# Performance work log

Measured on AMD Instinct MI355X. Metric: run time of the kernel, lower is better.

Reference implementation:

```python
import jax, jax.numpy as jnp
import numpy as np

N_NODES = 100000
N_EDGES = 1600000
F_IN = 512
D_EMB = 128
D_HID = 64
N_CLS = 32
EPS = 1e-5


def setup_inputs() -> dict:
    key = jax.random.key(0)
    ks = jax.random.split(key, 16)
    def w(k, shape):
        fan_in = shape[0]
        return jax.random.normal(k, shape, dtype=jnp.float32) / jnp.sqrt(jnp.float32(fan_in))
    return {
        "x": jax.random.normal(ks[0], (N_NODES, F_IN), dtype=jnp.float32),
        "W1": w(ks[1], (F_IN, D_EMB)), "b1": jnp.zeros((D_EMB,), jnp.float32),
        "Wc1": w(ks[2], (D_EMB, D_HID)), "bc1": jnp.zeros((D_HID,), jnp.float32),
        "Wc2": w(ks[3], (D_HID, D_HID)), "bc2": jnp.zeros((D_HID,), jnp.float32),
        "Wc3": w(ks[4], (D_HID, D_HID)), "bc3": jnp.zeros((D_HID,), jnp.float32),
        "gamma": jnp.ones((D_HID,), jnp.float32), "beta": jnp.zeros((D_HID,), jnp.float32),
        "W2": w(ks[5], (D_HID, N_CLS)), "b2": jnp.zeros((N_CLS,), jnp.float32),
        "W3": w(ks[6], (N_CLS, N_CLS)), "b3": jnp.zeros((N_CLS,), jnp.float32),
        "edge_index": jax.random.randint(ks[7], (2, N_EDGES), 0, N_NODES, dtype=jnp.int32),
    }


def _agg_mean(h, src, dst, n):
    # gather source-node features along edges, sum into destination nodes, divide by degree
    s = jax.ops.segment_sum(h[src], dst, num_segments=n)          # [N, d]
    deg = jax.ops.segment_sum(jnp.ones((src.shape[0], 1), h.dtype), dst, num_segments=n)
    return s / jnp.maximum(deg, 1.0)


def _conv1p(h, src, dst, W, b):
    # ConvolutionalLayer_1P: neighborhood gather/aggregate -> linear -> relu
    return jax.nn.relu(_agg_mean(h, src, dst, h.shape[0]) @ W + b)


def reference(x, W1, b1, Wc1, bc1, Wc2, bc2, Wc3, bc3, gamma, beta, W2, b2, W3, b3, edge_index):
    src, dst = edge_index[0], edge_index[1]
    # linmaps1 on 0th-order ptensors == identity copy
    h = jax.nn.relu(x @ W1 + b1)                 # lin1 + relu (dropout = identity in eval)
    h = _conv1p(h, src, dst, Wc1, bc1)           # conv1
    h = _conv1p(h, src, dst, Wc2, bc2)           # conv2
    h = _conv1p(h, src, dst, Wc3, bc3)           # conv3
    mean = jnp.mean(h, axis=0)
    var = jnp.var(h, axis=0)
    h = (h - mean) * jax.lax.rsqrt(var + EPS) * gamma + beta  # batchnorm (batch stats)
    h = jax.nn.relu(h @ W2 + b2)                 # lin2 + relu (dropout = identity)
    out = h @ W3 + b3                            # lin3; linmaps0 == identity
    return out
```

## Files before the change

kernel.cpp:

```cpp
#include <hip/hip_runtime.h>
#include <cstdint>
#include <cstddef>

constexpr int F_IN  = 512;
constexpr int D_EMB = 128;
constexpr int D_HID = 64;
constexpr int N_CLS = 32;

typedef __attribute__((ext_vector_type(8))) short short8;
typedef __attribute__((ext_vector_type(4))) float floatx4;

__device__ inline unsigned short f2bf(float f) {
  union { float f; uint32_t u; } v; v.f = f;
  uint32_t r = v.u + 0x7FFF + ((v.u >> 16) & 1);
  return (unsigned short)(r >> 16);
}

__global__ __launch_bounds__(256) void wt_kernel(
    const float* __restrict__ W1, short8* __restrict__ Wt2)
{
  int idx = blockIdx.x * 256 + threadIdx.x;
  int kc8 = idx >> 10, lin = idx & 1023;
  int ct = lin >> 7, rem = lin & 127, ks = rem >> 6, ln = rem & 63;
  int col = ct * 16 + (ln & 15);
  int k0 = kc8 * 64 + ks * 32 + (ln >> 4) * 8;
  short8 s;
#pragma unroll
  for (int j = 0; j < 8; ++j)
    s[j] = (short)f2bf(W1[(size_t)(k0 + j) * D_EMB + col]);
  Wt2[idx] = s;
}

__global__ __launch_bounds__(256) void l1c1_kernel(
    const float* __restrict__ X, const short8* __restrict__ Wt2,
    const float* __restrict__ b1, const float* __restrict__ Wc1,
    float* __restrict__ P, int n)
{
  __shared__ __align__(16) char smem[50176];
  short8* Xs = (short8*)smem;
  short8* Ws = (short8*)(smem + 8192);
  float (*Hs)[132] = (float(*)[132])smem;
  float (*Wc)[64]  = (float(*)[64])(smem + 33792);

  const int t = threadIdx.x;
  const int wave = t >> 6, lane = t & 63;
  const int quad = lane >> 4, mrow = lane & 15;
  const int node0 = blockIdx.x * 64;
  const int cw = wave * 2;

  float4 wp[4];
#pragma unroll
  for (int i = 0; i < 4; ++i) wp[i] = ((const float4*)Wc1)[i * 256 + t];

  const float* sp[2];
  int soff[2];
#pragma unroll
  for (int i = 0; i < 2; ++i) {
    int g = t + i * 256;
    int row = g >> 3, col8 = g & 7;
    soff[i] = row * 128 + ((col8 * 16) ^ ((row & 7) << 4));
    int gr = node0 + row; if (gr >= n) gr = n - 1;
    sp[i] = &X[(size_t)gr * F_IN + col8 * 8];
  }

  floatx4 acc[4][2];
#pragma unroll
  for (int i = 0; i < 4; ++i)
#pragma unroll
    for (int j = 0; j < 2; ++j) acc[i][j] = (floatx4){0.f, 0.f, 0.f, 0.f};

  float4 xrA[2][2], xrB[2][2];
  short8 wrA[4], wrB[4];

#pragma unroll
  for (int i = 0; i < 2; ++i) {
    xrA[i][0] = *(const float4*)sp[i];
    xrA[i][1] = *(const float4*)(sp[i] + 4);
    xrB[i][0] = *(const float4*)(sp[i] + 64);
    xrB[i][1] = *(const float4*)(sp[i] + 68);
  }
#pragma unroll
  for (int i = 0; i < 4; ++i) {
    wrA[i] = Wt2[t + i * 256];
    wrB[i] = Wt2[1024 + t + i * 256];
  }

  auto substep = [&](float4 (&xr)[2][2], short8 (&wr)[4], int knext) {
    short8 s8[2];
#pragma unroll
    for (int i = 0; i < 2; ++i) {
      s8[i][0] = (short)f2bf(xr[i][0].x); s8[i][1] = (short)f2bf(xr[i][0].y);
      s8[i][2] = (short)f2bf(xr[i][0].z); s8[i][3] = (short)f2bf(xr[i][0].w);
      s8[i][4] = (short)f2bf(xr[i][1].x); s8[i][5] = (short)f2bf(xr[i][1].y);
      s8[i][6] = (short)f2bf(xr[i][1].z); s8[i][7] = (short)f2bf(xr[i][1].w);
    }
    __syncthreads();
#pragma unroll
    for (int i = 0; i < 2; ++i)
      *(short8*)((char*)Xs + soff[i]) = s8[i];
#pragma unroll
    for (int i = 0; i < 4; ++i)
      Ws[t + i * 256] = wr[i];
    __syncthreads();

    if (knext < 8) {
#pragma unroll
      for (int i = 0; i < 2; ++i) {
        const float* p = sp[i] + knext * 64;
        xr[i][0] = *(const float4*)p;
        xr[i][1] = *(const float4*)(p + 4);
      }
#pragma unroll
      for (int i = 0; i < 4; ++i)
        wr[i] = Wt2[knext * 1024 + t + i * 256];
    }

#pragma unroll
    for (int ks = 0; ks < 2; ++ks) {
      short8 af[4], bf[2];
#pragma unroll
      for (int rt = 0; rt < 4; ++rt) {
        int row = rt * 16 + mrow;
        int byteoff = row * 128 + ((ks * 64 + quad * 16) ^ ((row & 7) << 4));
        af[rt] = *(const short8*)((const char*)Xs + byteoff);
      }
#pragma unroll
      for (int c = 0; c < 2; ++c)
        bf[c] = Ws[((cw + c) * 2 + ks) * 64 + lane];
#pragma unroll
      for (int rt = 0; rt < 4; ++rt)
#pragma unroll
        for (int c = 0; c < 2; ++c)
          acc[rt][c] = __builtin_amdgcn_mfma_f32_16x16x32_bf16(
              af[rt], bf[c], acc[rt][c], 0, 0, 0);
    }
  };

#pragma unroll 1
  for (int kc8 = 0; kc8 < 8; kc8 += 2) {
    substep(xrA, wrA, kc8 + 2);
    substep(xrB, wrB, kc8 + 3);
  }

  __syncthreads();
#pragma unroll
  for (int ct = 0; ct < 2; ++ct) {
    int col = (cw + ct) * 16 + mrow;
    float b = b1[col];
#pragma unroll
    for (int rt = 0; rt < 4; ++rt)
#pragma unroll
      for (int r = 0; r < 4; ++r)
        Hs[rt * 16 + quad * 4 + r][col] = fmaxf(acc[rt][ct][r] + b, 0.f);
  }
#pragma unroll
  for (int i = 0; i < 4; ++i)
    ((float4*)&Wc[0][0])[i * 256 + t] = wp[i];
  __syncthreads();

#pragma unroll
  for (int i = 0; i < 4; ++i)
    wp[i] = ((const float4*)Wc1)[1024 + i * 256 + t];

  const int rg = t >> 4, cg = t & 15;
  float acc2[4][4];
#pragma unroll
  for (int i = 0; i < 4; ++i)
#pragma unroll
    for (int j = 0; j < 4; ++j) acc2[i][j] = 0.f;

#pragma unroll 8
  for (int k = 0; k < 64; ++k) {
    float a[4] = {Hs[rg*4+0][k], Hs[rg*4+1][k], Hs[rg*4+2][k], Hs[rg*4+3][k]};
    float4 b = *(const float4*)&Wc[k][cg * 4];
#pragma unroll
    for (int i = 0; i < 4; ++i) {
      acc2[i][0] += a[i]*b.x; acc2[i][1] += a[i]*b.y;
      acc2[i][2] += a[i]*b.z; acc2[i][3] += a[i]*b.w;
    }
  }
  __syncthreads();
#pragma unroll
  for (int i = 0; i < 4; ++i)
    ((float4*)&Wc[0][0])[i * 256 + t] = wp[i];
  __syncthreads();

#pragma unroll 8
  for (int k = 0; k < 64; ++k) {
    float a[4] = {Hs[rg*4+0][64+k], Hs[rg*4+1][64+k],
                  Hs[rg*4+2][64+k], Hs[rg*4+3][64+k]};
    float4 b = *(const float4*)&Wc[k][cg * 4];
#pragma unroll
    for (int i = 0; i < 4; ++i) {
      acc2[i][0] += a[i]*b.x; acc2[i][1] += a[i]*b.y;
      acc2[i][2] += a[i]*b.z; acc2[i][3] += a[i]*b.w;
    }
  }
#pragma unroll
  for (int i = 0; i < 4; ++i) {
    int gn = node0 + rg * 4 + i;
    if (gn < n) {
      float4 o = make_float4(acc2[i][0], acc2[i][1], acc2[i][2], acc2[i][3]);
      *(float4*)&P[(size_t)gn * 64 + cg * 4] = o;
    }
  }
}

__device__ inline float gather_row(
    const float* __restrict__ P, const int* __restrict__ adj,
    int beg, int end, int lane)
{
  float a0=0.f,a1=0.f,a2=0.f,a3=0.f,a4=0.f,a5=0.f,a6=0.f,a7=0.f;
  int j = beg;
  for (; j + 8 <= end; j += 8) {
    int s0=adj[j+0], s1=adj[j+1], s2=adj[j+2], s3=adj[j+3];
    int s4=adj[j+4], s5=adj[j+5], s6=adj[j+6], s7=adj[j+7];
    a0 += P[(size_t)s0 * 64 + lane];
    a1 += P[(size_t)s1 * 64 + lane];
    a2 += P[(size_t)s2 * 64 + lane];
    a3 += P[(size_t)s3 * 64 + lane];
    a4 += P[(size_t)s4 * 64 + lane];
    a5 += P[(size_t)s5 * 64 + lane];
    a6 += P[(size_t)s6 * 64 + lane];
    a7 += P[(size_t)s7 * 64 + lane];
  }
  if (j < end) {
    int e1 = end - 1;
    int s0 = adj[j];
    int s1 = adj[min(j+1,e1)], s2 = adj[min(j+2,e1)], s3 = adj[min(j+3,e1)];
    int s4 = adj[min(j+4,e1)], s5 = adj[min(j+5,e1)], s6 = adj[min(j+6,e1)];
    float v0 = P[(size_t)s0 * 64 + lane];
    float v1 = P[(size_t)s1 * 64 + lane];
    float v2 = P[(size_t)s2 * 64 + lane];
    float v3 = P[(size_t)s3 * 64 + lane];
    float v4 = P[(size_t)s4 * 64 + lane];
    float v5 = P[(size_t)s5 * 64 + lane];
    float v6 = P[(size_t)s6 * 64 + lane];
    a0 += v0;
    a1 += (j+1 < end) ? v1 : 0.f;
    a2 += (j+2 < end) ? v2 : 0.f;
    a3 += (j+3 < end) ? v3 : 0.f;
    a4 += (j+4 < end) ? v4 : 0.f;
    a5 += (j+5 < end) ? v5 : 0.f;
    a6 += (j+6 < end) ? v6 : 0.f;
  }
  return ((a0+a1)+(a2+a3))+((a4+a5)+(a6+a7));
}

__global__ __launch_bounds__(512) void gmm_kernel(
    const float* __restrict__ P, const int* __restrict__ offs,
    const int* __restrict__ adj, const int* __restrict__ deg,
    const float* __restrict__ bin, const float* __restrict__ W,
    float* __restrict__ Out, int n)
{
  __shared__ float Hs[64][68];
  __shared__ float Ws[64][64];
  const int t = threadIdx.x;
  const int wave = t >> 6, lane = t & 63;
  const int node0 = blockIdx.x * 64;

#pragma unroll
  for (int i = 0; i < 2; ++i) {
    int lin = t + i * 512;
    ((float4*)&Ws[0][0])[lin] = ((const float4*)W)[lin];
  }
  const float bb = bin[lane];

#pragma unroll 1
  for (int nd = 0; nd < 8; ++nd) {
    int ln = wave * 8 + nd;
    int node = node0 + ln;
    float v = 0.f;
    if (node < n) {
      int beg = __builtin_amdgcn_readfirstlane(offs[node]);
      int end = __builtin_amdgcn_readfirstlane(offs[node + 1]);
      float s = gather_row(P, adj, beg, end, lane);
      float rd = 1.f / fmaxf((float)deg[node], 1.f);
      v = fmaxf(s * rd + bb, 0.f);
    }
    Hs[ln][lane] = v;
  }
  __syncthreads();

  const int rg = t >> 4, cg = t & 15;
  float acc[2][4];
#pragma unroll
  for (int i = 0; i < 2; ++i)
#pragma unroll
    for (int j = 0; j < 4; ++j) acc[i][j] = 0.f;

#pragma unroll 8
  for (int k = 0; k < 64; ++k) {
    float a[2] = {Hs[rg * 2 + 0][k], Hs[rg * 2 + 1][k]};
    float4 b = *(const float4*)&Ws[k][cg * 4];
#pragma unroll
    for (int i = 0; i < 2; ++i) {
      acc[i][0] += a[i]*b.x; acc[i][1] += a[i]*b.y;
      acc[i][2] += a[i]*b.z; acc[i][3] += a[i]*b.w;
    }
  }
#pragma unroll
  for (int i = 0; i < 2; ++i) {
    int gn = node0 + rg * 2 + i;
    if (gn < n) {
      float4 o = make_float4(acc[i][0], acc[i][1], acc[i][2], acc[i][3]);
      *(float4*)&Out[(size_t)gn * 64 + cg * 4] = o;
    }
  }
}

__global__ __launch_bounds__(512) void gp_kernel(
    const float* __restrict__ P, const int* __restrict__ offs,
    const int* __restrict__ adj, const int* __restrict__ deg,
    const float* __restrict__ bc3, float* __restrict__ H4,
    float* __restrict__ stats, int n)
{
  const int t = threadIdx.x;
  const int wave = t >> 6, lane = t & 63;
  const int node0 = blockIdx.x * 64;
  const float bb = bc3[lane];
  float s = 0.f, s2 = 0.f;

#pragma unroll 1
  for (int nd = 0; nd < 8; ++nd) {
    int node = node0 + wave * 8 + nd;
    if (node >= n) break;
    int beg = __builtin_amdgcn_readfirstlane(offs[node]);
    int end = __builtin_amdgcn_readfirstlane(offs[node + 1]);
    float a = gather_row(P, adj, beg, end, lane);
    float rd = 1.f / fmaxf((float)deg[node], 1.f);
    float v = fmaxf(a * rd + bb, 0.f);
    H4[(size_t)node * 64 + lane] = v;
    s += v; s2 += v * v;
  }

  __shared__ float red[2][8][64];
  red[0][wave][lane] = s; red[1][wave][lane] = s2;
  __syncthreads();
  if (t < 128) {
    int which = t >> 6, ff = t & 63;
    float a = 0.f;
#pragma unroll
    for (int w = 0; w < 8; ++w) a += red[which][w][ff];
    atomicAdd(&stats[which * 64 + ff], a);
  }
}

__global__ __launch_bounds__(256) void hist_kernel(
    const int* __restrict__ dst, int* __restrict__ G,
    float* __restrict__ stats, int nE, int B, int NB)
{
  __shared__ int h[256];
  int blk = blockIdx.x, t = threadIdx.x;
  if (blk == 0 && t < 128) stats[t] = 0.f;
  h[t] = 0;
  __syncthreads();
  int base = blk * 8192;
  int lim = min(8192, nE - base);
  for (int i = t; i < lim; i += 256)
    atomicAdd(&h[dst[base + i] >> 9], 1);
  __syncthreads();
  if (t < NB) G[t * B + blk] = h[t];
}

__global__ __launch_bounds__(256) void scan1_kernel(
    const int* __restrict__ in, int* __restrict__ out,
    int* __restrict__ bsum, int n)
{
  __shared__ int sh[256];
  int t = threadIdx.x;
  int i = blockIdx.x * 256 + t;
  int c = (i < n) ? in[i] : 0;
  sh[t] = c;
  __syncthreads();
#pragma unroll
  for (int off = 1; off < 256; off <<= 1) {
    int v = 0;
    if (t >= off) v = sh[t - off];
    __syncthreads();
    if (t >= off) sh[t] += v;
    __syncthreads();
  }
  if (i < n) out[i] = sh[t] - c;
  if (t == 255) bsum[blockIdx.x] = sh[255];
}

__global__ __launch_bounds__(256) void scan2_kernel(int* __restrict__ bsum, int nb)
{
  __shared__ int sh[256];
  __shared__ int carry;
  int t = threadIdx.x;
  if (t == 0) carry = 0;
  __syncthreads();
  for (int base = 0; base < nb; base += 256) {
    int i = base + t;
    int v = (i < nb) ? bsum[i] : 0;
    sh[t] = v;
    __syncthreads();
#pragma unroll
    for (int off = 1; off < 256; off <<= 1) {
      int u = 0;
      if (t >= off) u = sh[t - off];
      __syncthreads();
      if (t >= off) sh[t] += u;
      __syncthreads();
    }
    int c0 = carry;
    int incl = sh[t], total = sh[255];
    if (i < nb) bsum[i] = c0 + incl - v;
    __syncthreads();
    if (t == 0) carry = c0 + total;
    __syncthreads();
  }
  if (t == 0) bsum[nb] = carry;
}

__global__ __launch_bounds__(256) void scatter2_kernel(
    const int* __restrict__ src, const int* __restrict__ dst,
    const int* __restrict__ W, const int* __restrict__ bsum,
    int2* __restrict__ EP, int nE, int B, int NB)
{
  __shared__ int cur[256];
  int blk = blockIdx.x, t = threadIdx.x;
  if (t < NB) {
    int gi = t * B + blk;
    cur[t] = W[gi] + bsum[gi >> 8];
  }
  __syncthreads();
  int base = blk * 8192;
  int lim = min(8192, nE - base);
  for (int i = t; i < lim; i += 256) {
    int s = src[base + i], d = dst[base + i];
    int slot = atomicAdd(&cur[d >> 9], 1);
    EP[slot] = make_int2(s, d);
  }
}

__global__ __launch_bounds__(256) void fillc_kernel(
    const int2* __restrict__ EP, const int* __restrict__ W,
    const int* __restrict__ bsum,
    int* __restrict__ cnt, int* __restrict__ offs, int* __restrict__ adj,
    int n, int nE, int B, int NB)
{
  __shared__ int h[512];
  int b = blockIdx.x, t = threadIdx.x;
  int g0i = b * B;
  int segStart = W[g0i] + bsum[g0i >> 8];
  int segEnd = (b == NB - 1) ? nE : (W[g0i + B] + bsum[(g0i + B) >> 8]);
  int nodeBase = b << 9;

  h[t] = 0; h[t + 256] = 0;
  __syncthreads();
  for (int i = segStart + t; i < segEnd; i += 256)
    atomicAdd(&h[EP[i].y - nodeBase], 1);
  __syncthreads();
  int c0 = h[t], c1 = h[t + 256];
#pragma unroll
  for (int off = 1; off < 512; off <<= 1) {
    int a = (t >= off) ? h[t - off] : 0;
    int bb = (t + 256 >= off) ? h[t + 256 - off] : 0;
    __syncthreads();
    h[t] += a; h[t + 256] += bb;
    __syncthreads();
  }
  int e0 = h[t] - c0, e1 = h[t + 256] - c1;
  int g0 = nodeBase + t, g1 = nodeBase + t + 256;
  if (g0 < n) { cnt[g0] = c0; offs[g0] = segStart + e0; }
  if (g1 < n) { cnt[g1] = c1; offs[g1] = segStart + e1; }
  if (b == 0 && t == 0) offs[n] = nE;
  __syncthreads();
  h[t] = e0; h[t + 256] = e1;
  __syncthreads();
  for (int i = segStart + t; i < segEnd; i += 256) {
    int2 p = EP[i];
    int slot = atomicAdd(&h[p.y - nodeBase], 1);
    adj[segStart + slot] = p.x;
  }
}

__global__ __launch_bounds__(256) void fold_kernel(
    const float* __restrict__ stats, const float* __restrict__ gamma,
    const float* __restrict__ beta, const float* __restrict__ W2,
    const float* __restrict__ b2, float* __restrict__ W2f,
    float* __restrict__ b2f, int n)
{
  __shared__ float rsg[64], corr[64];
  int t = threadIdx.x;
  if (t < 64) {
    float m = stats[t] / (float)n;
    float var = stats[64 + t] / (float)n - m * m;
    float rs = rsqrtf(var + 1e-5f);
    float g = gamma[t] * rs;
    rsg[t] = g;
    corr[t] = beta[t] - m * g;
  }
  __syncthreads();
#pragma unroll
  for (int i = 0; i < 8; ++i) {
    int lin = t + i * 256;
    int k = lin >> 5;
    W2f[lin] = rsg[k] * W2[lin];
  }
  if (t < 32) {
    float a = b2[t];
    for (int k = 0; k < 64; ++k) a += corr[k] * W2[k * 32 + t];
    b2f[t] = a;
  }
}

__global__ __launch_bounds__(256) void final_kernel(
    const float* __restrict__ H4, const float* __restrict__ W2f,
    const float* __restrict__ b2f, const float* __restrict__ W3,
    const float* __restrict__ b3, float* __restrict__ Out, int n)
{
  __shared__ float Hs[64][68];
  __shared__ float W2s[64][32];
  __shared__ float W3s[32][32];
  __shared__ float Us[64][36];
  __shared__ float b2s[32], b3s[32];
  const int t = threadIdx.x;
  const int node0 = blockIdx.x * 64;

#pragma unroll
  for (int i = 0; i < 4; ++i) {
    int lin = t + i * 256;
    int node = lin >> 4, kq = lin & 15;
    float4 v = make_float4(0.f, 0.f, 0.f, 0.f);
    if (node0 + node < n)
      v = *(const float4*)&H4[(size_t)(node0 + node) * 64 + kq * 4];
    *(float4*)&Hs[node][kq * 4] = v;
  }
#pragma unroll
  for (int i = 0; i < 2; ++i) {
    int lin = t + i * 256;
    ((float4*)&W2s[0][0])[lin] = ((const float4*)W2f)[lin];
  }
  ((float4*)&W3s[0][0])[t & 255] = ((const float4*)W3)[t & 255];
  if (t < 32) { b2s[t] = b2f[t]; b3s[t] = b3[t]; }
  __syncthreads();

  const int rg = t >> 4, cg = t & 15;
  float acc[4][2] = {{0.f,0.f},{0.f,0.f},{0.f,0.f},{0.f,0.f}};
#pragma unroll 8
  for (int k = 0; k < 64; ++k) {
    float a[4] = {Hs[rg*4+0][k], Hs[rg*4+1][k], Hs[rg*4+2][k], Hs[rg*4+3][k]};
    float w0 = W2s[k][cg*2], w1 = W2s[k][cg*2+1];
#pragma unroll
    for (int i = 0; i < 4; ++i) { acc[i][0] += a[i]*w0; acc[i][1] += a[i]*w1; }
  }
#pragma unroll
  for (int i = 0; i < 4; ++i) {
    Us[rg*4+i][cg*2+0] = fmaxf(acc[i][0] + b2s[cg*2+0], 0.f);
    Us[rg*4+i][cg*2+1] = fmaxf(acc[i][1] + b2s[cg*2+1], 0.f);
  }
  __syncthreads();

  float acc2[4][2] = {{0.f,0.f},{0.f,0.f},{0.f,0.f},{0.f,0.f}};
#pragma unroll
  for (int k = 0; k < 32; ++k) {
    float a[4] = {Us[rg*4+0][k], Us[rg*4+1][k], Us[rg*4+2][k], Us[rg*4+3][k]};
    float w0 = W3s[k][cg*2], w1 = W3s[k][cg*2+1];
#pragma unroll
    for (int i = 0; i < 4; ++i) { acc2[i][0] += a[i]*w0; acc2[i][1] += a[i]*w1; }
  }
  float (*Os)[36] = (float(*)[36])Hs;
#pragma unroll
  for (int i = 0; i < 4; ++i) {
    Os[rg*4+i][cg*2+0] = acc2[i][0] + b3s[cg*2+0];
    Os[rg*4+i][cg*2+1] = acc2[i][1] + b3s[cg*2+1];
  }
  __syncthreads();
#pragma unroll
  for (int i = 0; i < 2; ++i) {
    int lin = t + i * 256;
    int node = lin >> 3, c4 = lin & 7;
    if (node0 + node < n)
      *(float4*)&Out[(size_t)(node0 + node) * 32 + c4 * 4] =
          *(float4*)&Os[node][c4 * 4];
  }
}

extern "C" void kernel_launch(void* const* d_in, const int* in_sizes, int n_in,
                              void* d_out, int out_size, void* d_ws, size_t ws_size,
                              hipStream_t stream)
{
  const float* X     = (const float*)d_in[0];
  const float* W1    = (const float*)d_in[1];
  const float* b1    = (const float*)d_in[2];
  const float* Wc1   = (const float*)d_in[3];
  const float* bc1   = (const float*)d_in[4];
  const float* Wc2   = (const float*)d_in[5];
  const float* bc2   = (const float*)d_in[6];
  const float* Wc3   = (const float*)d_in[7];
  const float* bc3   = (const float*)d_in[8];
  const float* gamma = (const float*)d_in[9];
  const float* beta  = (const float*)d_in[10];
  const float* W2    = (const float*)d_in[11];
  const float* b2    = (const float*)d_in[12];
  const float* W3    = (const float*)d_in[13];
  const float* b3    = (const float*)d_in[14];
  const int*   ei    = (const int*)d_in[15];

  const int n  = in_sizes[0] / F_IN;
  const int nE = in_sizes[15] / 2;
  const int* src  = ei;
  const int* dstv = ei + nE;

  const int NB = (n + 511) >> 9;
  const int B  = (nE + 8191) >> 13;
  const int NG = NB * B;
  const int nbG = (NG + 255) / 256;

  float* ws    = (float*)d_ws;
  float* Pa    = ws;
  float* Pb    = Pa + (size_t)n * D_HID;
  float* stats = Pb + (size_t)n * D_HID;
  float* W2f   = stats + 128;
  float* b2f   = W2f + 2048;
  int*   cnt   = (int*)(b2f + 32);
  int*   offs  = cnt + n;
  int*   G     = offs + n + 1;
  int*   W     = G + NG;
  int*   bsum  = W + NG + 1;
  int*   adj   = bsum + nbG + 1;
  uintptr_t epAddr = ((uintptr_t)(adj + nE) + 7) & ~(uintptr_t)7;
  int2*  EP    = (int2*)epAddr;
  short8* Wt2  = (short8*)(EP + nE);
  float* H4    = Pb;

  const int nb  = (n + 63) / 64;

  wt_kernel<<<32, 256, 0, stream>>>(W1, Wt2);
  l1c1_kernel<<<nb, 256, 0, stream>>>(X, Wt2, b1, Wc1, Pa, n);

  hist_kernel<<<B, 256, 0, stream>>>(dstv, G, stats, nE, B, NB);
  scan1_kernel<<<nbG, 256, 0, stream>>>(G, W, bsum, NG);
  scan2_kernel<<<1, 256, 0, stream>>>(bsum, nbG);
  scatter2_kernel<<<B, 256, 0, stream>>>(src, dstv, W, bsum, EP, nE, B, NB);
  fillc_kernel<<<NB, 256, 0, stream>>>(EP, W, bsum, cnt, offs, adj, n, nE, B, NB);

  gmm_kernel<<<nb, 512, 0, stream>>>(Pa, offs, adj, cnt, bc1, Wc2, Pb, n);

  gmm_kernel<<<nb, 512, 0, stream>>>(Pb, offs, adj, cnt, bc2, Wc3, Pa, n);

  gp_kernel<<<nb, 512, 0, stream>>>(Pa, offs, adj, cnt, bc3, H4, stats, n);

  fold_kernel<<<1, 256, 0, stream>>>(stats, gamma, beta, W2, b2, W2f, b2f, n);
  final_kernel<<<nb, 256, 0, stream>>>(H4, W2f, b2f, W3, b3, (float*)d_out, n);
}
```

Baseline: 632.0 us.

## Store intermediate node features as bf16 and split gathers across half-waves

The projected node features feeding the first two aggregation passes are now stored in bf16, which halves the bytes moved by the random per-edge gathers. Each gather now has two half-waves take alternate edges, with each lane loading two features, and the partial sums are combined with a cross-lane shuffle. The CSR offsets for each block are staged in shared memory. The third pass keeps fp32 input, so the workspace layout changes. The cost is bf16 rounding error in the intermediate activations, which could affect accuracy tolerance.

```diff
diff --git a/kernel.cpp b/kernel.cpp
--- a/kernel.cpp
+++ b/kernel.cpp
@@ -14,6 +14,10 @@
   union { float f; uint32_t u; } v; v.f = f;
   uint32_t r = v.u + 0x7FFF + ((v.u >> 16) & 1);
   return (unsigned short)(r >> 16);
+}
+
+__device__ inline uint32_t pack2bf(float lo, float hi) {
+  return ((uint32_t)f2bf(hi) << 16) | (uint32_t)f2bf(lo);
 }
 
 __global__ __launch_bounds__(256) void wt_kernel(
@@ -34,7 +38,7 @@
 __global__ __launch_bounds__(256) void l1c1_kernel(
     const float* __restrict__ X, const short8* __restrict__ Wt2,
     const float* __restrict__ b1, const float* __restrict__ Wc1,
-    float* __restrict__ P, int n)
+    unsigned short* __restrict__ P, int n)
 {
   __shared__ __align__(16) char smem[50176];
   short8* Xs = (short8*)smem;
@@ -200,63 +204,75 @@
   for (int i = 0; i < 4; ++i) {
     int gn = node0 + rg * 4 + i;
     if (gn < n) {
-      float4 o = make_float4(acc2[i][0], acc2[i][1], acc2[i][2], acc2[i][3]);
-      *(float4*)&P[(size_t)gn * 64 + cg * 4] = o;
-    }
-  }
-}
-
-__device__ inline float gather_row(
+      uint2 o;
+      o.x = pack2bf(acc2[i][0], acc2[i][1]);
+      o.y = pack2bf(acc2[i][2], acc2[i][3]);
+      *(uint2*)&P[(size_t)gn * 64 + cg * 4] = o;
+    }
+  }
+}
+
+__device__ inline void gather2_bf(
+    const unsigned short* __restrict__ P, const int* __restrict__ adj,
+    int beg, int end, int g, int li, float& c0, float& c1)
+{
+  c0 = 0.f; c1 = 0.f;
+  if (end <= beg) return;
+  int e1 = end - 1;
+  for (int jj = beg + g; jj < end; jj += 16) {
+#pragma unroll
+    for (int k = 0; k < 8; ++k) {
+      int e = jj + 2 * k;
+      int ec = min(e, e1);
+      int idx = adj[ec];
+      uint32_t u = *(const uint32_t*)&P[(size_t)idx * 64 + li * 2];
+      float lo = __uint_as_float(u << 16);
+      float hi = __uint_as_float(u & 0xFFFF0000u);
+      bool p = e < end;
+      c0 += p ? lo : 0.f;
+      c1 += p ? hi : 0.f;
+    }
+  }
+  c0 += __shfl_xor(c0, 32, 64);
+  c1 += __shfl_xor(c1, 32, 64);
+}
+
+__device__ inline void gather2_f32(
     const float* __restrict__ P, const int* __restrict__ adj,
-    int beg, int end, int lane)
-{
-  float a0=0.f,a1=0.f,a2=0.f,a3=0.f,a4=0.f,a5=0.f,a6=0.f,a7=0.f;
-  int j = beg;
-  for (; j + 8 <= end; j += 8) {
-    int s0=adj[j+0], s1=adj[j+1], s2=adj[j+2], s3=adj[j+3];
-    int s4=adj[j+4], s5=adj[j+5], s6=adj[j+6], s7=adj[j+7];
-    a0 += P[(size_t)s0 * 64 + lane];
-    a1 += P[(size_t)s1 * 64 + lane];
-    a2 += P[(size_t)s2 * 64 + lane];
-    a3 += P[(size_t)s3 * 64 + lane];
-    a4 += P[(size_t)s4 * 64 + lane];
-    a5 += P[(size_t)s5 * 64 + lane];
-    a6 += P[(size_t)s6 * 64 + lane];
-    a7 += P[(size_t)s7 * 64 + lane];
-  }
-  if (j < end) {
-    int e1 = end - 1;
-    int s0 = adj[j];
-    int s1 = adj[min(j+1,e1)], s2 = adj[min(j+2,e1)], s3 = adj[min(j+3,e1)];
-    int s4 = adj[min(j+4,e1)], s5 = adj[min(j+5,e1)], s6 = adj[min(j+6,e1)];
-    float v0 = P[(size_t)s0 * 64 + lane];
-    float v1 = P[(size_t)s1 * 64 + lane];
-    float v2 = P[(size_t)s2 * 64 + lane];
-    float v3 = P[(size_t)s3 * 64 + lane];
-    float v4 = P[(size_t)s4 * 64 + lane];
-    float v5 = P[(size_t)s5 * 64 + lane];
-    float v6 = P[(size_t)s6 * 64 + lane];
-    a0 += v0;
-    a1 += (j+1 < end) ? v1 : 0.f;
-    a2 += (j+2 < end) ? v2 : 0.f;
-    a3 += (j+3 < end) ? v3 : 0.f;
-    a4 += (j+4 < end) ? v4 : 0.f;
-    a5 += (j+5 < end) ? v5 : 0.f;
-    a6 += (j+6 < end) ? v6 : 0.f;
-  }
-  return ((a0+a1)+(a2+a3))+((a4+a5)+(a6+a7));
-}
-
+    int beg, int end, int g, int li, float& c0, float& c1)
+{
+  c0 = 0.f; c1 = 0.f;
+  if (end <= beg) return;
+  int e1 = end - 1;
+  for (int jj = beg + g; jj < end; jj += 16) {
+#pragma unroll
+    for (int k = 0; k < 8; ++k) {
+      int e = jj + 2 * k;
+      int ec = min(e, e1);
+      int idx = adj[ec];
+      float2 u = *(const float2*)&P[(size_t)idx * 64 + li * 2];
+      bool p = e < end;
+      c0 += p ? u.x : 0.f;
+      c1 += p ? u.y : 0.f;
+    }
+  }
+  c0 += __shfl_xor(c0, 32, 64);
+  c1 += __shfl_xor(c1, 32, 64);
+}
+
+template<bool INBF, bool OUTBF>
 __global__ __launch_bounds__(512) void gmm_kernel(
-    const float* __restrict__ P, const int* __restrict__ offs,
+    const void* __restrict__ Pv, const int* __restrict__ offs,
     const int* __restrict__ adj, const int* __restrict__ deg,
     const float* __restrict__ bin, const float* __restrict__ W,
-    float* __restrict__ Out, int n)
+    void* __restrict__ Outv, int n)
 {
   __shared__ float Hs[64][68];
   __shared__ float Ws[64][64];
+  __shared__ int offss[65];
   const int t = threadIdx.x;
   const int wave = t >> 6, lane = t & 63;
+  const int g = lane >> 5, li = lane & 31;
   const int node0 = blockIdx.x * 64;
 
 #pragma unroll
@@ -264,21 +280,30 @@
     int lin = t + i * 512;
     ((float4*)&Ws[0][0])[lin] = ((const float4*)W)[lin];
   }
-  const float bb = bin[lane];
+  if (t < 65) offss[t] = offs[min(node0 + t, n)];
+  __syncthreads();
+
+  const float2 bb = *(const float2*)&bin[li * 2];
 
 #pragma unroll 1
   for (int nd = 0; nd < 8; ++nd) {
     int ln = wave * 8 + nd;
     int node = node0 + ln;
-    float v = 0.f;
     if (node < n) {
-      int beg = __builtin_amdgcn_readfirstlane(offs[node]);
-      int end = __builtin_amdgcn_readfirstlane(offs[node + 1]);
-      float s = gather_row(P, adj, beg, end, lane);
+      float c0, c1;
+      if (INBF)
+        gather2_bf((const unsigned short*)Pv, adj, offss[ln], offss[ln + 1],
+                   g, li, c0, c1);
+      else
+        gather2_f32((const float*)Pv, adj, offss[ln], offss[ln + 1],
+                    g, li, c0, c1);
       float rd = 1.f / fmaxf((float)deg[node], 1.f);
-      v = fmaxf(s * rd + bb, 0.f);
-    }
-    Hs[ln][lane] = v;
+      float v0 = fmaxf(c0 * rd + bb.x, 0.f);
+      float v1 = fmaxf(c1 * rd + bb.y, 0.f);
+      if (g == 0) *(float2*)&Hs[ln][li * 2] = make_float2(v0, v1);
+    } else if (g == 0) {
+      *(float2*)&Hs[ln][li * 2] = make_float2(0.f, 0.f);
+    }
   }
   __syncthreads();
 
@@ -303,8 +328,15 @@
   for (int i = 0; i < 2; ++i) {
     int gn = node0 + rg * 2 + i;
     if (gn < n) {
-      float4 o = make_float4(acc[i][0], acc[i][1], acc[i][2], acc[i][3]);
-      *(float4*)&Out[(size_t)gn * 64 + cg * 4] = o;
+      if (OUTBF) {
+        uint2 o;
+        o.x = pack2bf(acc[i][0], acc[i][1]);
+        o.y = pack2bf(acc[i][2], acc[i][3]);
+        *(uint2*)&((unsigned short*)Outv)[(size_t)gn * 64 + cg * 4] = o;
+      } else {
+        float4 o = make_float4(acc[i][0], acc[i][1], acc[i][2], acc[i][3]);
+        *(float4*)&((float*)Outv)[(size_t)gn * 64 + cg * 4] = o;
+      }
     }
   }
 }
@@ -315,27 +347,36 @@
     const float* __restrict__ bc3, float* __restrict__ H4,
     float* __restrict__ stats, int n)
 {
+  __shared__ int offss[65];
   const int t = threadIdx.x;
   const int wave = t >> 6, lane = t & 63;
+  const int g = lane >> 5, li = lane & 31;
   const int node0 = blockIdx.x * 64;
-  const float bb = bc3[lane];
-  float s = 0.f, s2 = 0.f;
+  if (t < 65) offss[t] = offs[min(node0 + t, n)];
+  __syncthreads();
+
+  const float2 bb = *(const float2*)&bc3[li * 2];
+  float s0 = 0.f, s1 = 0.f, q0 = 0.f, q1 = 0.f;
 
 #pragma unroll 1
   for (int nd = 0; nd < 8; ++nd) {
-    int node = node0 + wave * 8 + nd;
+    int ln = wave * 8 + nd;
+    int node = node0 + ln;
     if (node >= n) break;
-    int beg = __builtin_amdgcn_readfirstlane(offs[node]);
-    int end = __builtin_amdgcn_readfirstlane(offs[node + 1]);
-    float a = gather_row(P, adj, beg, end, lane);
+    float c0, c1;
+    gather2_f32(P, adj, offss[ln], offss[ln + 1], g, li, c0, c1);
     float rd = 1.f / fmaxf((float)deg[node], 1.f);
-    float v = fmaxf(a * rd + bb, 0.f);
-    H4[(size_t)node * 64 + lane] = v;
-    s += v; s2 += v * v;
+    float v0 = fmaxf(c0 * rd + bb.x, 0.f);
+    float v1 = fmaxf(c1 * rd + bb.y, 0.f);
+    if (g == 0) *(float2*)&H4[(size_t)node * 64 + li * 2] = make_float2(v0, v1);
+    s0 += v0; s1 += v1; q0 += v0 * v0; q1 += v1 * v1;
   }
 
   __shared__ float red[2][8][64];
-  red[0][wave][lane] = s; red[1][wave][lane] = s2;
+  if (g == 0) {
+    red[0][wave][li * 2 + 0] = s0; red[0][wave][li * 2 + 1] = s1;
+    red[1][wave][li * 2 + 0] = q0; red[1][wave][li * 2 + 1] = q1;
+  }
   __syncthreads();
   if (t < 128) {
     int which = t >> 6, ff = t & 63;
@@ -611,10 +652,12 @@
   const int NG = NB * B;
   const int nbG = (NG + 255) / 256;
 
-  float* ws    = (float*)d_ws;
-  float* Pa    = ws;
-  float* Pb    = Pa + (size_t)n * D_HID;
-  float* stats = Pb + (size_t)n * D_HID;
+  char* wsb = (char*)d_ws;
+  unsigned short* Pa = (unsigned short*)wsb;
+  unsigned short* Pb = (unsigned short*)(wsb + (size_t)n * 128);
+  float* Pc    = (float*)(wsb + (size_t)n * 256);
+  float* H4    = (float*)(wsb + (size_t)n * 512);
+  float* stats = H4 + (size_t)n * 64;
   float* W2f   = stats + 128;
   float* b2f   = W2f + 2048;
   int*   cnt   = (int*)(b2f + 32);
@@ -626,7 +669,6 @@
   uintptr_t epAddr = ((uintptr_t)(adj + nE) + 7) & ~(uintptr_t)7;
   int2*  EP    = (int2*)epAddr;
   short8* Wt2  = (short8*)(EP + nE);
-  float* H4    = Pb;
 
   const int nb  = (n + 63) / 64;
 
@@ -639,11 +681,13 @@
   scatter2_kernel<<<B, 256, 0, stream>>>(src, dstv, W, bsum, EP, nE, B, NB);
   fillc_kernel<<<NB, 256, 0, stream>>>(EP, W, bsum, cnt, offs, adj, n, nE, B, NB);
 
-  gmm_kernel<<<nb, 512, 0, stream>>>(Pa, offs, adj, cnt, bc1, Wc2, Pb, n);
-
-  gmm_kernel<<<nb, 512, 0, stream>>>(Pb, offs, adj, cnt, bc2, Wc3, Pa, n);
-
-  gp_kernel<<<nb, 512, 0, stream>>>(Pa, offs, adj, cnt, bc3, H4, stats, n);
+  gmm_kernel<true, true><<<nb, 512, 0, stream>>>(
+      Pa, offs, adj, cnt, bc1, Wc2, Pb, n);
+
+  gmm_kernel<true, false><<<nb, 512, 0, stream>>>(
+      Pb, offs, adj, cnt, bc2, Wc3, Pc, n);
+
+  gp_kernel<<<nb, 512, 0, stream>>>(Pc, offs, adj, cnt, bc3, H4, stats, n);
 
   fold_kernel<<<1, 256, 0, stream>>>(stats, gamma, beta, W2, b2, W2f, b2f, n);
   final_kernel<<<nb, 256, 0, stream>>>(H4, W2f, b2f, W3, b3, (float*)d_out, n);
```

Result: faster. 601.1 us (-4.9%).
